# Kernel optimization log

Measured on AMD Instinct MI355X. Metric: run time of the kernel, lower is better.

The kernel has to match this reference:

```python
import jax, jax.numpy as jnp
import numpy as np

DIST_THD = 2.0  # squared-distance threshold from my_chamfer_fn


def setup_inputs() -> dict:
    key = jax.random.key(0)
    k1, k2 = jax.random.split(key)
    pc1 = jax.random.normal(k1, (1, 16384, 3), dtype=jnp.float32)
    pc2 = jax.random.normal(k2, (1, 16384, 3), dtype=jnp.float32)
    return {"pc1": pc1, "pc2": pc2}


def _chamfer(x, y):
    # x: (N, P1, D), y: (N, P2, D). Squared pairwise distances (as pytorch3d knn_points).
    x2 = jnp.sum(x * x, axis=-1)                       # (N, P1)
    y2 = jnp.sum(y * y, axis=-1)                       # (N, P2)
    xy = jnp.einsum('npd,nqd->npq', x, y)              # (N, P1, P2)
    d2 = x2[:, :, None] + y2[:, None, :] - 2.0 * xy    # (N, P1, P2)
    cham_x = jnp.min(d2, axis=2)                       # (N, P1) NN dist x->y (K=1)
    cham_y = jnp.min(d2, axis=1)                       # (N, P2) NN dist y->x
    # threshold mask: distances >= 2 are zeroed
    cham_x = jnp.where(cham_x >= DIST_THD, 0.0, cham_x)
    cham_y = jnp.where(cham_y >= DIST_THD, 0.0, cham_y)
    N, P1, _ = x.shape
    P2 = y.shape[1]
    # point_reduction='mean' (lengths are full P), batch_reduction='mean'
    cx = jnp.sum(cham_x, axis=1) / P1
    cy = jnp.sum(cham_y, axis=1) / P2
    return jnp.sum(cx) / N + jnp.sum(cy) / N


def reference(pc1, pc2):
    # Chamfer loss between pc1 and pc2 (the kernel inside NSFP optimization);
    # normals are unused in this code path, so only the distance loss is returned.
    return _chamfer(pc1, pc2)
```

## Files before the change

kernel.cpp:

```cpp
#include <hip/hip_runtime.h>
#include <hip/hip_bf16.h>


constexpr int P      = 16384;
constexpr int BLK    = 256;
constexpr int XPT    = 8;
constexpr int XCHUNK = BLK * XPT;
constexpr int YSPLIT = 32;
constexpr int YSEG   = P / YSPLIT;

typedef float v2f __attribute__((ext_vector_type(2)));

static __device__ inline v2f pk_fma(v2f a, v2f b, v2f c) {
    v2f d;
    asm("v_pk_fma_f32 %0, %1, %2, %3" : "=v"(d) : "v"(a), "v"(b), "v"(c));
    return d;
}

__global__ __launch_bounds__(BLK) void chamfer_main(
    const float* __restrict__ pc1, const float* __restrict__ pc2,
    float* __restrict__ partial,
    float* __restrict__ out)
{
    if (blockIdx.x == 0 && blockIdx.y == 0 && blockIdx.z == 0 && threadIdx.x == 0)
        out[0] = 0.0f;

    const int dir = blockIdx.z;
    const float* xs = dir ? pc2 : pc1;
    const float* ys = dir ? pc1 : pc2;

    __shared__ __align__(16) float ytX[YSEG], ytY[YSEG], ytZ[YSEG], ytW[YSEG];
    const int ybase = blockIdx.y * YSEG;
    for (int k = threadIdx.x; k < YSEG; k += BLK) {
        const int q = ybase + k;
        const float a = ys[3 * q], b = ys[3 * q + 1], c = ys[3 * q + 2];
        ytX[k] = a; ytY[k] = b; ytZ[k] = c;
        ytW[k] = -0.5f * fmaf(a, a, fmaf(b, b, c * c));
    }

    const int p0 = blockIdx.x * XCHUNK + threadIdx.x;
    v2f xs0[XPT], xs1[XPT], xs2[XPT];
    float acc[XPT];
    #pragma unroll
    for (int k = 0; k < XPT; ++k) {
        const int p = p0 + k * BLK;
        const float a = xs[3 * p], b = xs[3 * p + 1], c = xs[3 * p + 2];
        xs0[k] = (v2f){a, a};
        xs1[k] = (v2f){b, b};
        xs2[k] = (v2f){c, c};
        acc[k] = -3.0e38f;
    }
    __syncthreads();

    #pragma unroll 2
    for (int jp = 0; jp < YSEG / 2; ++jp) {
        const v2f y0 = *(const v2f*)&ytX[2 * jp];
        const v2f y1 = *(const v2f*)&ytY[2 * jp];
        const v2f y2 = *(const v2f*)&ytZ[2 * jp];
        const v2f yw = *(const v2f*)&ytW[2 * jp];
        #pragma unroll
        for (int k = 0; k < XPT; ++k) {
            v2f t = pk_fma(xs0[k], y0, yw);
            t = pk_fma(xs1[k], y1, t);
            t = pk_fma(xs2[k], y2, t);
            acc[k] = fmaxf(fmaxf(acc[k], t.x), t.y);
        }
    }

    float* pout = partial + ((size_t)dir * YSPLIT + blockIdx.y) * P;
    #pragma unroll
    for (int k = 0; k < XPT; ++k) pout[p0 + k * BLK] = acc[k];
}

__global__ __launch_bounds__(BLK) void chamfer_reduce(
    const float* __restrict__ partial,
    const float* __restrict__ pc1, const float* __restrict__ pc2,
    float* __restrict__ out)
{
    const int gid = blockIdx.x * BLK + threadIdx.x;
    const int dir = (gid >= P) ? 1 : 0;
    const int p = gid & (P - 1);
    const float* xsrc = dir ? pc2 : pc1;
    const float* base = partial + (size_t)dir * YSPLIT * P + p;

    float M = base[0];
    #pragma unroll
    for (int s = 1; s < YSPLIT; ++s) M = fmaxf(M, base[(size_t)s * P]);

    const float a = xsrc[3 * p], b = xsrc[3 * p + 1], c = xsrc[3 * p + 2];
    const float xx = fmaf(a, a, fmaf(b, b, c * c));
    float d2 = fmaf(-2.0f, M, xx);
    if (d2 >= 2.0f) d2 = 0.0f;
    float v = d2 * (1.0f / (float)P);

    #pragma unroll
    for (int off = 32; off > 0; off >>= 1) v += __shfl_down(v, off, 64);

    __shared__ float wsum[BLK / 64];
    const int lane = threadIdx.x & 63;
    const int wv = threadIdx.x >> 6;
    if (lane == 0) wsum[wv] = v;
    __syncthreads();
    if (threadIdx.x == 0) {
        float s = wsum[0];
        #pragma unroll
        for (int w = 1; w < BLK / 64; ++w) s += wsum[w];
        atomicAdd(out, s);
    }
}

extern "C" void kernel_launch(void* const* d_in, const int* in_sizes, int n_in,
                              void* d_out, int out_size, void* d_ws, size_t ws_size,
                              hipStream_t stream) {
    const float* pc1 = (const float*)d_in[0];
    const float* pc2 = (const float*)d_in[1];
    float* out = (float*)d_out;
    float* partial = (float*)d_ws;

    dim3 grid(P / XCHUNK, YSPLIT, 2);
    chamfer_main<<<grid, BLK, 0, stream>>>(pc1, pc2, partial, out);
    chamfer_reduce<<<(2 * P) / BLK, BLK, 0, stream>>>(partial, pc1, pc2, out);
}
```

Before: 103.8 us.

## Raise y-split and shrink per-thread tile, interleave LDS layout, use max3

Halves points per thread and doubles the y-split so four times as many blocks cover the GPU. The y tile in shared memory is interleaved so each pair of y points is fetched with two float4 loads. The two max ops are fused into v_max3_f32. The cost is twice as many partial maxima written and read by the reduce kernel, and more LDS reuse overhead per block.

```diff
diff --git a/kernel.cpp b/kernel.cpp
--- a/kernel.cpp
+++ b/kernel.cpp
@@ -4,10 +4,11 @@
 
 constexpr int P      = 16384;
 constexpr int BLK    = 256;
-constexpr int XPT    = 8;
+constexpr int XPT    = 4;
 constexpr int XCHUNK = BLK * XPT;
-constexpr int YSPLIT = 32;
+constexpr int YSPLIT = 64;
 constexpr int YSEG   = P / YSPLIT;
+constexpr int NGRP   = YSEG / 2;
 
 typedef float v2f __attribute__((ext_vector_type(2)));
 
@@ -16,8 +17,13 @@
     asm("v_pk_fma_f32 %0, %1, %2, %3" : "=v"(d) : "v"(a), "v"(b), "v"(c));
     return d;
 }
+static __device__ inline float max3(float a, float b, float c) {
+    float d;
+    asm("v_max3_f32 %0, %1, %2, %3" : "=v"(d) : "v"(a), "v"(b), "v"(c));
+    return d;
+}
 
-__global__ __launch_bounds__(BLK) void chamfer_main(
+__global__ __launch_bounds__(BLK, 4) void chamfer_main(
     const float* __restrict__ pc1, const float* __restrict__ pc2,
     float* __restrict__ partial,
     float* __restrict__ out)
@@ -29,13 +35,17 @@
     const float* xs = dir ? pc2 : pc1;
     const float* ys = dir ? pc1 : pc2;
 
-    __shared__ __align__(16) float ytX[YSEG], ytY[YSEG], ytZ[YSEG], ytW[YSEG];
-    const int ybase = blockIdx.y * YSEG;
-    for (int k = threadIdx.x; k < YSEG; k += BLK) {
-        const int q = ybase + k;
+    __shared__ __align__(16) float yt[NGRP * 8];
+    {
+        const int j = threadIdx.x;
+        const int q = blockIdx.y * YSEG + j;
         const float a = ys[3 * q], b = ys[3 * q + 1], c = ys[3 * q + 2];
-        ytX[k] = a; ytY[k] = b; ytZ[k] = c;
-        ytW[k] = -0.5f * fmaf(a, a, fmaf(b, b, c * c));
+        const int g = j >> 1, par = j & 1;
+        float* gp = &yt[g * 8 + par];
+        gp[0] = a;
+        gp[2] = b;
+        gp[4] = c;
+        gp[6] = -0.5f * fmaf(a, a, fmaf(b, b, c * c));
     }
 
     const int p0 = blockIdx.x * XCHUNK + threadIdx.x;
@@ -52,18 +62,21 @@
     }
     __syncthreads();
 
+    const float4* gptr = (const float4*)yt;
     #pragma unroll 2
-    for (int jp = 0; jp < YSEG / 2; ++jp) {
-        const v2f y0 = *(const v2f*)&ytX[2 * jp];
-        const v2f y1 = *(const v2f*)&ytY[2 * jp];
-        const v2f y2 = *(const v2f*)&ytZ[2 * jp];
-        const v2f yw = *(const v2f*)&ytW[2 * jp];
+    for (int g = 0; g < NGRP; ++g) {
+        const float4 A = gptr[2 * g];
+        const float4 B = gptr[2 * g + 1];
+        const v2f y0 = {A.x, A.y};
+        const v2f y1 = {A.z, A.w};
+        const v2f y2 = {B.x, B.y};
+        const v2f yw = {B.z, B.w};
         #pragma unroll
         for (int k = 0; k < XPT; ++k) {
             v2f t = pk_fma(xs0[k], y0, yw);
             t = pk_fma(xs1[k], y1, t);
             t = pk_fma(xs2[k], y2, t);
-            acc[k] = fmaxf(fmaxf(acc[k], t.x), t.y);
+            acc[k] = max3(acc[k], t.x, t.y);
         }
     }
 
```

Measured after the change: 99.78 us. 3.8% less time.

## Compute pairwise distances with bf16 MFMA using split hi/lo encoding

Applied to the files above, without the earlier changes.

Replaces the packed-FP32 FMA distance loop with 32x32x16 bf16 MFMA instructions. Each point is encoded as hi/lo bf16 pairs plus its squared norm, so one matrix product yields the full squared distance, and the cross terms keep close to fp32 accuracy. The y tiles are encoded into shared memory in rounds, the min is accumulated per MFMA output and reduced across lanes with shuffles, and the y split drops from 32 to 8 segments. The extra encoding work and the reduced precision of the split-bf16 scheme could change results near the distance threshold.

```diff
diff --git a/kernel.cpp b/kernel.cpp
--- a/kernel.cpp
+++ b/kernel.cpp
@@ -4,22 +4,67 @@
 
 constexpr int P      = 16384;
 constexpr int BLK    = 256;
-constexpr int XPT    = 8;
-constexpr int XCHUNK = BLK * XPT;
-constexpr int YSPLIT = 32;
-constexpr int YSEG   = P / YSPLIT;
+constexpr int NSEG   = 8;
+constexpr int SEGPTS = P / NSEG;
+constexpr int ROUND  = 1024;
+constexpr int TILES  = ROUND / 32;
+constexpr int ROWSB  = 256;
 
-typedef float v2f __attribute__((ext_vector_type(2)));
+typedef short s8v  __attribute__((ext_vector_type(8)));
+typedef float f16v __attribute__((ext_vector_type(16)));
 
-static __device__ inline v2f pk_fma(v2f a, v2f b, v2f c) {
-    v2f d;
-    asm("v_pk_fma_f32 %0, %1, %2, %3" : "=v"(d) : "v"(a), "v"(b), "v"(c));
-    return d;
+static __device__ inline unsigned short bf16r(float f) {
+    unsigned u = __float_as_uint(f);
+    u = (u + 0x7FFFu + ((u >> 16) & 1u)) >> 16;
+    return (unsigned short)u;
+}
+static __device__ inline float bf2f(unsigned short h) {
+    return __uint_as_float(((unsigned)h) << 16);
 }
 
-__global__ __launch_bounds__(BLK) void chamfer_main(
+static __device__ inline void encA(float a, float b, float c, unsigned e[8]) {
+    const unsigned ONE = 0x3F80u;
+    const float s = fmaf(a, a, fmaf(b, b, c * c));
+    const unsigned short ah = bf16r(a), bh = bf16r(b), ch = bf16r(c);
+    const unsigned short al = bf16r(a - bf2f(ah));
+    const unsigned short bl = bf16r(b - bf2f(bh));
+    const unsigned short cl = bf16r(c - bf2f(ch));
+    const unsigned short sh = bf16r(s), sl = bf16r(s - bf2f(sh));
+    e[0] = ah | ((unsigned)al << 16);
+    e[1] = bh | ((unsigned)bl << 16);
+    e[2] = ch | ((unsigned)cl << 16);
+    e[3] = ah | ((unsigned)bh << 16);
+    e[4] = ch | ((unsigned)sh << 16);
+    e[5] = sl | (ONE << 16);
+    e[6] = ONE;
+    e[7] = 0;
+}
+
+static __device__ inline void encB(float a, float b, float c, unsigned e[8]) {
+    const unsigned ONE = 0x3F80u;
+    const float s = fmaf(a, a, fmaf(b, b, c * c));
+    const unsigned short ah = bf16r(a), bh = bf16r(b), ch = bf16r(c);
+    const unsigned short al = bf16r(a - bf2f(ah));
+    const unsigned short bl = bf16r(b - bf2f(bh));
+    const unsigned short cl = bf16r(c - bf2f(ch));
+    const unsigned short sh = bf16r(s), sl = bf16r(s - bf2f(sh));
+    const unsigned short Ah = bf16r(-2.f * bf2f(ah)), Bh = bf16r(-2.f * bf2f(bh));
+    const unsigned short Ch = bf16r(-2.f * bf2f(ch));
+    const unsigned short Al = bf16r(-2.f * bf2f(al)), Bl = bf16r(-2.f * bf2f(bl));
+    const unsigned short Cl = bf16r(-2.f * bf2f(cl));
+    e[0] = Ah | ((unsigned)Ah << 16);
+    e[1] = Bh | ((unsigned)Bh << 16);
+    e[2] = Ch | ((unsigned)Ch << 16);
+    e[3] = Al | ((unsigned)Bl << 16);
+    e[4] = Cl | (ONE << 16);
+    e[5] = ONE | ((unsigned)sh << 16);
+    e[6] = sl;
+    e[7] = 0;
+}
+
+__global__ __launch_bounds__(BLK, 4) void chamfer_mfma(
     const float* __restrict__ pc1, const float* __restrict__ pc2,
-    float* __restrict__ partial,
+    float* __restrict__ part,
     float* __restrict__ out)
 {
     if (blockIdx.x == 0 && blockIdx.y == 0 && blockIdx.z == 0 && threadIdx.x == 0)
@@ -29,83 +74,103 @@
     const float* xs = dir ? pc2 : pc1;
     const float* ys = dir ? pc1 : pc2;
 
-    __shared__ __align__(16) float ytX[YSEG], ytY[YSEG], ytZ[YSEG], ytW[YSEG];
-    const int ybase = blockIdx.y * YSEG;
-    for (int k = threadIdx.x; k < YSEG; k += BLK) {
-        const int q = ybase + k;
-        const float a = ys[3 * q], b = ys[3 * q + 1], c = ys[3 * q + 2];
-        ytX[k] = a; ytY[k] = b; ytZ[k] = c;
-        ytW[k] = -0.5f * fmaf(a, a, fmaf(b, b, c * c));
+    __shared__ __align__(16) unsigned char ytile[ROUND * 32];
+
+    const int tid  = threadIdx.x;
+    const int lane = tid & 63;
+    const int wv   = tid >> 6;
+    const int l31  = lane & 31;
+    const int half = lane >> 5;
+
+    const int rowbase = blockIdx.x * ROWSB + wv * 64;
+    s8v afrag[2];
+    #pragma unroll
+    for (int s = 0; s < 2; ++s) {
+        const int p = rowbase + s * 32 + l31;
+        unsigned e[8];
+        encA(xs[3 * p], xs[3 * p + 1], xs[3 * p + 2], e);
+        union { uint4 i; s8v v; } lo, hi;
+        lo.i = make_uint4(e[0], e[1], e[2], e[3]);
+        hi.i = make_uint4(e[4], e[5], e[6], e[7]);
+        afrag[s] = half ? hi.v : lo.v;
     }
 
-    const int p0 = blockIdx.x * XCHUNK + threadIdx.x;
-    v2f xs0[XPT], xs1[XPT], xs2[XPT];
-    float acc[XPT];
+    f16v acc0, acc1, Z;
     #pragma unroll
-    for (int k = 0; k < XPT; ++k) {
-        const int p = p0 + k * BLK;
-        const float a = xs[3 * p], b = xs[3 * p + 1], c = xs[3 * p + 2];
-        xs0[k] = (v2f){a, a};
-        xs1[k] = (v2f){b, b};
-        xs2[k] = (v2f){c, c};
-        acc[k] = -3.0e38f;
+    for (int i = 0; i < 16; ++i) { acc0[i] = 3.0e38f; acc1[i] = 3.0e38f; Z[i] = 0.0f; }
+
+    const int segbase = blockIdx.y * SEGPTS;
+    for (int r = 0; r < SEGPTS / ROUND; ++r) {
+        #pragma unroll 2
+        for (int j = 0; j < ROUND / BLK; ++j) {
+            const int i = tid + j * BLK;
+            const int q = segbase + r * ROUND + i;
+            unsigned e[8];
+            encB(ys[3 * q], ys[3 * q + 1], ys[3 * q + 2], e);
+            const int tt = i >> 5, cc = i & 31;
+            *(uint4*)(ytile + tt * 1024 +       cc * 16) = make_uint4(e[0], e[1], e[2], e[3]);
+            *(uint4*)(ytile + tt * 1024 + 512 + cc * 16) = make_uint4(e[4], e[5], e[6], e[7]);
+        }
+        __syncthreads();
+
+        const unsigned char* rp = ytile + lane * 16;
+        #pragma unroll 2
+        for (int t = 0; t < TILES; ++t) {
+            const s8v bfrag = *(const s8v*)(rp + t * 1024);
+            const f16v d0 = __builtin_amdgcn_mfma_f32_32x32x16_bf16(afrag[0], bfrag, Z, 0, 0, 0);
+            acc0 = __builtin_elementwise_min(acc0, d0);
+            const f16v d1 = __builtin_amdgcn_mfma_f32_32x32x16_bf16(afrag[1], bfrag, Z, 0, 0, 0);
+            acc1 = __builtin_elementwise_min(acc1, d1);
+        }
+        __syncthreads();
     }
-    __syncthreads();
 
-    #pragma unroll 2
-    for (int jp = 0; jp < YSEG / 2; ++jp) {
-        const v2f y0 = *(const v2f*)&ytX[2 * jp];
-        const v2f y1 = *(const v2f*)&ytY[2 * jp];
-        const v2f y2 = *(const v2f*)&ytZ[2 * jp];
-        const v2f yw = *(const v2f*)&ytW[2 * jp];
+    float* pbase = part + ((size_t)(dir * NSEG + blockIdx.y)) * P;
+    #pragma unroll
+    for (int s = 0; s < 2; ++s) {
         #pragma unroll
-        for (int k = 0; k < XPT; ++k) {
-            v2f t = pk_fma(xs0[k], y0, yw);
-            t = pk_fma(xs1[k], y1, t);
-            t = pk_fma(xs2[k], y2, t);
-            acc[k] = fmaxf(fmaxf(acc[k], t.x), t.y);
+        for (int rg = 0; rg < 16; ++rg) {
+            float v = s ? acc1[rg] : acc0[rg];
+            v = fminf(v, __shfl_xor(v, 1, 64));
+            v = fminf(v, __shfl_xor(v, 2, 64));
+            v = fminf(v, __shfl_xor(v, 4, 64));
+            v = fminf(v, __shfl_xor(v, 8, 64));
+            v = fminf(v, __shfl_xor(v, 16, 64));
+            if (l31 == 0) {
+                const int row = rowbase + s * 32 + (rg & 3) + 8 * (rg >> 2) + 4 * half;
+                pbase[row] = v;
+            }
         }
     }
-
-    float* pout = partial + ((size_t)dir * YSPLIT + blockIdx.y) * P;
-    #pragma unroll
-    for (int k = 0; k < XPT; ++k) pout[p0 + k * BLK] = acc[k];
 }
 
 __global__ __launch_bounds__(BLK) void chamfer_reduce(
-    const float* __restrict__ partial,
-    const float* __restrict__ pc1, const float* __restrict__ pc2,
-    float* __restrict__ out)
+    const float* __restrict__ part, float* __restrict__ out)
 {
     const int gid = blockIdx.x * BLK + threadIdx.x;
-    const int dir = (gid >= P) ? 1 : 0;
-    const int p = gid & (P - 1);
-    const float* xsrc = dir ? pc2 : pc1;
-    const float* base = partial + (size_t)dir * YSPLIT * P + p;
+    const int dirbase = (gid >= P) ? NSEG * P : 0;
+    const int row = gid & (P - 1);
 
-    float M = base[0];
+    float m = part[dirbase + row];
     #pragma unroll
-    for (int s = 1; s < YSPLIT; ++s) M = fmaxf(M, base[(size_t)s * P]);
+    for (int s = 1; s < NSEG; ++s) m = fminf(m, part[dirbase + s * P + row]);
 
-    const float a = xsrc[3 * p], b = xsrc[3 * p + 1], c = xsrc[3 * p + 2];
-    const float xx = fmaf(a, a, fmaf(b, b, c * c));
-    float d2 = fmaf(-2.0f, M, xx);
-    if (d2 >= 2.0f) d2 = 0.0f;
-    float v = d2 * (1.0f / (float)P);
+    if (m >= 2.0f) m = 0.0f;
+    float v = m * (1.0f / (float)P);
 
     #pragma unroll
     for (int off = 32; off > 0; off >>= 1) v += __shfl_down(v, off, 64);
 
     __shared__ float wsum[BLK / 64];
     const int lane = threadIdx.x & 63;
-    const int wv = threadIdx.x >> 6;
-    if (lane == 0) wsum[wv] = v;
+    const int wvi = threadIdx.x >> 6;
+    if (lane == 0) wsum[wvi] = v;
     __syncthreads();
     if (threadIdx.x == 0) {
-        float s = wsum[0];
+        float ssum = wsum[0];
         #pragma unroll
-        for (int w = 1; w < BLK / 64; ++w) s += wsum[w];
-        atomicAdd(out, s);
+        for (int w = 1; w < BLK / 64; ++w) ssum += wsum[w];
+        atomicAdd(out, ssum);
     }
 }
 
@@ -115,9 +180,9 @@
     const float* pc1 = (const float*)d_in[0];
     const float* pc2 = (const float*)d_in[1];
     float* out = (float*)d_out;
-    float* partial = (float*)d_ws;
+    float* part = (float*)d_ws;
 
-    dim3 grid(P / XCHUNK, YSPLIT, 2);
-    chamfer_main<<<grid, BLK, 0, stream>>>(pc1, pc2, partial, out);
-    chamfer_reduce<<<(2 * P) / BLK, BLK, 0, stream>>>(partial, pc1, pc2, out);
+    dim3 grid(P / ROWSB, NSEG, 2);
+    chamfer_mfma<<<grid, BLK, 0, stream>>>(pc1, pc2, part, out);
+    chamfer_reduce<<<(2 * P) / BLK, BLK, 0, stream>>>(part, out);
 }
```

Result: faster. 84.18 us (-18.9%).
